# Kernel optimization log

Measured on AMD Instinct MI355X. Metric: run time of the kernel, lower is better.

The kernel has to match this reference:

```python
import jax, jax.numpy as jnp
import numpy as np

D_MODEL = 1024
N_HEADS = 16
D_HEAD = 64


def setup_inputs() -> dict:
    key = jax.random.key(0)
    ks = jax.random.split(key, 5)
    B, T = 2, 2048
    scale = 1.0 / np.sqrt(D_MODEL)
    x = jax.random.normal(ks[0], (B, T, D_MODEL), dtype=jnp.float32)
    Wq = jax.random.normal(ks[1], (N_HEADS * D_HEAD, D_MODEL), dtype=jnp.float32) * scale
    Wk = jax.random.normal(ks[2], (N_HEADS * D_HEAD, D_MODEL), dtype=jnp.float32) * scale
    Wv = jax.random.normal(ks[3], (N_HEADS * D_HEAD, D_MODEL), dtype=jnp.float32) * scale
    Wo = jax.random.normal(ks[4], (D_MODEL, N_HEADS * D_HEAD), dtype=jnp.float32) * scale
    return {"x": x, "Wq": Wq, "Wk": Wk, "Wv": Wv, "Wo": Wo}


def reference(x, Wq, Wk, Wv, Wo):
    B, T, D = x.shape
    # Linear(y = x @ W.T), then split heads: [B, H, T, d]
    def split_heads(y):
        return y.reshape(B, T, N_HEADS, D_HEAD).transpose(0, 2, 1, 3)
    q = split_heads(x @ Wq.T)
    k = split_heads(x @ Wk.T)
    v = split_heads(x @ Wv.T)
    scale = D_HEAD ** -0.5
    # Materialized [B, H, T, T] scores, as in the original module
    scores = jnp.einsum('bhtd,bhTd->bhtT', q, k) * scale
    attn = jax.nn.softmax(scores, axis=-1)
    y = jnp.einsum('bhtT,bhTd->bhtd', attn, v)
    y = y.transpose(0, 2, 1, 3).reshape(B, T, N_HEADS * D_HEAD)
    return y @ Wo.T
```

## Files before the change

### kernel.cpp

```cpp
#include <hip/hip_runtime.h>
#include <hip/hip_bf16.h>

typedef __attribute__((ext_vector_type(8))) short bf16x8;
typedef __attribute__((ext_vector_type(4))) float f32x4;
typedef unsigned short u16t;

#define DEVINL static __device__ __forceinline__

DEVINL u16t f2bf(float f) {
  union { __hip_bfloat16 h; u16t u; } cv;
  cv.h = __float2bfloat16(f);
  return cv.u;
}

DEVINL unsigned cvt_pk_bf16(float a, float b) {
  unsigned r;
  asm("v_cvt_pk_bf16_f32 %0, %1, %2" : "=v"(r) : "v"(a), "v"(b));
  return r;
}

DEVINL void async16(void* lds, const void* g) {
  __builtin_amdgcn_global_load_lds((const __attribute__((address_space(1))) void*)g,
                                   (__attribute__((address_space(3))) void*)lds,
                                   16, 0, 0);
}

__global__ __launch_bounds__(256) void convert_bf16(
    const float* __restrict__ x,  const float* __restrict__ wq,
    const float* __restrict__ wk, const float* __restrict__ wv,
    const float* __restrict__ wo,
    u16t* __restrict__ xb, u16t* __restrict__ wqb, u16t* __restrict__ wkb,
    u16t* __restrict__ wvb, u16t* __restrict__ wob) {
  const int blk = blockIdx.x;
  const float* src; u16t* dst; size_t off;
  if (blk < 4096)      { src = x;  dst = xb;  off = (size_t)blk * 1024; }
  else if (blk < 5120) { src = wq; dst = wqb; off = (size_t)(blk - 4096) * 1024; }
  else if (blk < 6144) { src = wk; dst = wkb; off = (size_t)(blk - 5120) * 1024; }
  else if (blk < 7168) { src = wv; dst = wvb; off = (size_t)(blk - 6144) * 1024; }
  else                 { src = wo; dst = wob; off = (size_t)(blk - 7168) * 1024; }
  const size_t i = off + (size_t)threadIdx.x * 4;
  const float4 v = *(const float4*)&src[i];
  ushort4 r;
  r.x = f2bf(v.x); r.y = f2bf(v.y); r.z = f2bf(v.z); r.w = f2bf(v.w);
  *(ushort4*)&dst[i] = r;
}

template <int MODE, int BM>
__global__ __launch_bounds__(256) void gemm_bt(
    const u16t* __restrict__ A, const u16t* __restrict__ B,
    void* __restrict__ C0, void* __restrict__ C1, void* __restrict__ C2,
    int M, int N, int K) {
  constexpr int MI = BM / 32;
  __shared__ u16t As[2][BM * 32];
  __shared__ u16t Bs[2][128 * 32];

  const int tid = threadIdx.x;
  const int lane = tid & 63;
  const int w = tid >> 6;
  const int wm = w >> 1, wn = w & 1;
  const int quad = lane >> 4, cl = lane & 15;
  const int m0 = blockIdx.y * BM;
  const int n0 = blockIdx.x * 128;

  const int srow = lane >> 2;
  const int scol = (lane & 3) * 8;

  f32x4 acc[MI][4] = {};

  #define STAGEP(b, kp)                                                       \
    {                                                                         \
      _Pragma("unroll")                                                       \
      for (int ii = 0; ii < BM / 64; ++ii) {                                  \
        const int c = w + ii * 4;                                             \
        async16(&As[b][c * 512],                                              \
                &A[(size_t)(m0 + c * 16 + srow) * K + (kp) * 32 + scol]);     \
      }                                                                       \
      _Pragma("unroll")                                                       \
      for (int ii = 0; ii < 2; ++ii) {                                        \
        const int c = w + ii * 4;                                             \
        async16(&Bs[b][c * 512],                                              \
                &B[(size_t)(n0 + c * 16 + srow) * K + (kp) * 32 + scol]);     \
      }                                                                       \
    }

  #define COMPUTEP(b)                                                         \
    {                                                                         \
      bf16x8 af[MI], bfr[4];                                                  \
      _Pragma("unroll")                                                       \
      for (int i = 0; i < MI; ++i)                                            \
        af[i] = *(const bf16x8*)&As[b][(wm * (BM / 2) + i * 16 + cl) * 32 + quad * 8]; \
      _Pragma("unroll")                                                       \
      for (int j = 0; j < 4; ++j)                                             \
        bfr[j] = *(const bf16x8*)&Bs[b][(wn * 64 + j * 16 + cl) * 32 + quad * 8]; \
      _Pragma("unroll")                                                       \
      for (int i = 0; i < MI; ++i)                                            \
        _Pragma("unroll")                                                     \
        for (int j = 0; j < 4; ++j)                                           \
          acc[i][j] = __builtin_amdgcn_mfma_f32_16x16x32_bf16(af[i], bfr[j], acc[i][j], 0, 0, 0); \
    }

  const int NP = K >> 5;
  STAGEP(0, 0);
  __syncthreads();
  for (int kp = 0; kp < NP; kp += 2) {
    if (kp + 1 < NP) STAGEP(1, kp + 1);
    COMPUTEP(0);
    __syncthreads();
    if (kp + 2 < NP) STAGEP(0, kp + 2);
    COMPUTEP(1);
    __syncthreads();
  }
  #undef STAGEP
  #undef COMPUTEP

  const int nz = n0 >> 10;
  #pragma unroll
  for (int i = 0; i < MI; ++i)
    #pragma unroll
    for (int j = 0; j < 4; ++j) {
      const int mb = m0 + wm * (BM / 2) + i * 16 + quad * 4;
      const int n  = n0 + wn * 64 + j * 16 + cl;
      if (MODE == 0) {
        #pragma unroll
        for (int r = 0; r < 4; ++r)
          ((float*)C0)[(size_t)(mb + r) * N + n] = acc[i][j][r];
      } else {
        const int nw = n & 1023, h = nw >> 6, d = nw & 63;
        const int b = mb >> 11, tb = mb & 2047;
        const size_t bh = (size_t)(b * 16 + h);
        if (nz == 2) {
          ushort4 v4;
          v4.x = f2bf(acc[i][j][0]); v4.y = f2bf(acc[i][j][1]);
          v4.z = f2bf(acc[i][j][2]); v4.w = f2bf(acc[i][j][3]);
          const size_t addr = (bh << 17) +
              (size_t)(((d >> 4) * 256 + (tb >> 3)) * 128 + (d & 15) * 8 + (tb & 7));
          *(ushort4*)&((u16t*)C2)[addr] = v4;
        } else if (nz == 1) {
          const size_t basea = (bh << 17) +
              (size_t)(((tb >> 4) * 8 + (d >> 3)) * 128 + (d & 7));
          #pragma unroll
          for (int r = 0; r < 4; ++r)
            ((u16t*)C1)[basea + ((tb & 15) + r) * 8] = f2bf(acc[i][j][r]);
        } else {
          #pragma unroll
          for (int r = 0; r < 4; ++r)
            ((u16t*)C0)[(bh * 2048 + tb + r) * 64 + d] =
                f2bf(acc[i][j][r] * 0.18033688011112043f);
        }
      }
    }
}

__global__ __launch_bounds__(256, 2) void flash_attn(
    const u16t* __restrict__ Q, const u16t* __restrict__ Kt,
    const u16t* __restrict__ Vt, u16t* __restrict__ Y) {
  __shared__ u16t Ps[4 * 32 * 136];
  const int tid = threadIdx.x;
  const int lane = tid & 63;
  const int w = tid >> 6;
  const int quad = lane >> 4, cl = lane & 15;
  const int bh = blockIdx.x;
  const int q0 = blockIdx.y * 128 + w * 32;
  const u16t* Kb = Kt + ((size_t)bh << 17);
  const u16t* Vb = Vt + ((size_t)bh << 17);

  bf16x8 aq[2][2];
  #pragma unroll
  for (int h = 0; h < 2; ++h)
    #pragma unroll
    for (int ks = 0; ks < 2; ++ks)
      aq[h][ks] = *(const bf16x8*)&Q[((size_t)bh * 2048 + q0 + 16 * h + cl) * 64 + ks * 32 + quad * 8];

  bf16x8 ones8;
  #pragma unroll
  for (int i = 0; i < 8; ++i) ones8[i] = (short)0x3F80;

  f32x4 o[2][4] = {};
  f32x4 psum[2] = {};

  u16t* Pw = &Ps[w * 32 * 136];

  for (int jt = 0; jt < 16; ++jt) {
    const int j0 = jt * 128;

    bf16x8 kf[2][8];
    #pragma unroll
    for (int ks = 0; ks < 2; ++ks)
      #pragma unroll
      for (int js = 0; js < 8; ++js)
        kf[ks][js] = *(const bf16x8*)&Kb[(size_t)((((j0 >> 4) + js) * 8 + ks * 4) * 128) + lane * 8];
    __builtin_amdgcn_sched_barrier(0);

    f32x4 s0[8] = {}, s1[8] = {};
    __builtin_amdgcn_s_setprio(1);
    #pragma unroll
    for (int ks = 0; ks < 2; ++ks) {
      #pragma unroll
      for (int js = 0; js < 8; ++js)
        s0[js] = __builtin_amdgcn_mfma_f32_16x16x32_bf16(kf[ks][js], aq[0][ks], s0[js], 0, 0, 0);
      #pragma unroll
      for (int js = 0; js < 8; ++js)
        s1[js] = __builtin_amdgcn_mfma_f32_16x16x32_bf16(kf[ks][js], aq[1][ks], s1[js], 0, 0, 0);
    }
    __builtin_amdgcn_s_setprio(0);

    bf16x8 vf[4][4];
    #pragma unroll
    for (int ks = 0; ks < 4; ++ks)
      #pragma unroll
      for (int ds = 0; ds < 4; ++ds)
        vf[ks][ds] = *(const bf16x8*)&Vb[(size_t)((ds * 256 + (j0 >> 3) + ks * 4) * 128) + lane * 8];
    __builtin_amdgcn_sched_barrier(0);

    #pragma unroll
    for (int js = 0; js < 8; ++js) {
      uint2 pk0, pk1;
      pk0.x = cvt_pk_bf16(__builtin_exp2f(s0[js][0]), __builtin_exp2f(s0[js][1]));
      pk0.y = cvt_pk_bf16(__builtin_exp2f(s0[js][2]), __builtin_exp2f(s0[js][3]));
      *(uint2*)&Pw[cl * 136 + js * 16 + quad * 4] = pk0;
      pk1.x = cvt_pk_bf16(__builtin_exp2f(s1[js][0]), __builtin_exp2f(s1[js][1]));
      pk1.y = cvt_pk_bf16(__builtin_exp2f(s1[js][2]), __builtin_exp2f(s1[js][3]));
      *(uint2*)&Pw[(16 + cl) * 136 + js * 16 + quad * 4] = pk1;
    }

    __builtin_amdgcn_s_setprio(1);
    #pragma unroll
    for (int ks = 0; ks < 4; ++ks) {
      const bf16x8 ap0 = *(const bf16x8*)&Pw[cl * 136 + ks * 32 + quad * 8];
      const bf16x8 ap1 = *(const bf16x8*)&Pw[(16 + cl) * 136 + ks * 32 + quad * 8];
      psum[0] = __builtin_amdgcn_mfma_f32_16x16x32_bf16(ap0, ones8, psum[0], 0, 0, 0);
      psum[1] = __builtin_amdgcn_mfma_f32_16x16x32_bf16(ap1, ones8, psum[1], 0, 0, 0);
      #pragma unroll
      for (int ds = 0; ds < 4; ++ds) {
        o[0][ds] = __builtin_amdgcn_mfma_f32_16x16x32_bf16(ap0, vf[ks][ds], o[0][ds], 0, 0, 0);
        o[1][ds] = __builtin_amdgcn_mfma_f32_16x16x32_bf16(ap1, vf[ks][ds], o[1][ds], 0, 0, 0);
      }
    }
    __builtin_amdgcn_s_setprio(0);
  }

  const int b = bh >> 4, hd = bh & 15;
  #pragma unroll
  for (int h = 0; h < 2; ++h) {
    float inv[4];
    #pragma unroll
    for (int r = 0; r < 4; ++r) inv[r] = __builtin_amdgcn_rcpf(psum[h][r]);
    #pragma unroll
    for (int ds = 0; ds < 4; ++ds)
      #pragma unroll
      for (int r = 0; r < 4; ++r) {
        const int t = q0 + 16 * h + quad * 4 + r;
        const int d = ds * 16 + cl;
        Y[((size_t)b * 2048 + t) * 1024 + hd * 64 + d] = f2bf(o[h][ds][r] * inv[r]);
      }
  }
}

extern "C" void kernel_launch(void* const* d_in, const int* in_sizes, int n_in,
                              void* d_out, int out_size, void* d_ws, size_t ws_size,
                              hipStream_t stream) {
  (void)in_sizes; (void)n_in; (void)out_size; (void)ws_size;
  const float* x  = (const float*)d_in[0];
  const float* Wq = (const float*)d_in[1];
  const float* Wk = (const float*)d_in[2];
  const float* Wv = (const float*)d_in[3];
  const float* Wo = (const float*)d_in[4];

  char* ws = (char*)d_ws;
  const size_t MB = 1024 * 1024;
  u16t* xb  = (u16t*)(ws);
  u16t* Wqb = (u16t*)(ws + 8 * MB);
  u16t* Wkb = (u16t*)(ws + 10 * MB);
  u16t* Wvb = (u16t*)(ws + 12 * MB);
  u16t* Wob = (u16t*)(ws + 14 * MB);
  u16t* Qw  = (u16t*)(ws + 16 * MB);
  u16t* Ktw = (u16t*)(ws + 24 * MB);
  u16t* Vtw = (u16t*)(ws + 32 * MB);
  u16t* Yw  = xb;

  convert_bf16<<<8192, 256, 0, stream>>>(x, Wq, Wk, Wv, Wo, xb, Wqb, Wkb, Wvb, Wob);
  gemm_bt<1, 128><<<dim3(24, 32), 256, 0, stream>>>(
      xb, Wqb, Qw, Ktw, Vtw, 4096, 3072, 1024);
  flash_attn<<<dim3(32, 16), 256, 0, stream>>>(Qw, Ktw, Vtw, Yw);
  gemm_bt<0, 64><<<dim3(8, 64), 256, 0, stream>>>(
      Yw, Wob, d_out, d_out, d_out, 4096, 1024, 1024);
}
```

Baseline: 196.1 us.

## Pre-swizzle QKV GEMM operands into fragment layout and load directly without LDS

The conversion kernel now writes x and the concatenated Wq/Wk/Wv in a 16-row by 8-element tiled layout that matches the MFMA fragment order, and does more work per block. A new QKV GEMM kernel reads its fragments straight from global memory with 16-byte loads, with no LDS staging or barriers, and asks for higher occupancy through its launch bounds. This removes shared-memory traffic and synchronization from the projection GEMM, but it relies on L1/L2 caching to supply operand reuse and has no software prefetch across k-steps.

```diff
diff --git a/kernel.cpp b/kernel.cpp
--- a/kernel.cpp
+++ b/kernel.cpp
@@ -2,6 +2,7 @@
 #include <hip/hip_bf16.h>
 
 typedef __attribute__((ext_vector_type(8))) short bf16x8;
+typedef __attribute__((ext_vector_type(8))) unsigned short u16x8;
 typedef __attribute__((ext_vector_type(4))) float f32x4;
 typedef unsigned short u16t;
 
@@ -29,20 +30,104 @@
     const float* __restrict__ x,  const float* __restrict__ wq,
     const float* __restrict__ wk, const float* __restrict__ wv,
     const float* __restrict__ wo,
-    u16t* __restrict__ xb, u16t* __restrict__ wqb, u16t* __restrict__ wkb,
-    u16t* __restrict__ wvb, u16t* __restrict__ wob) {
+    u16t* __restrict__ xb, u16t* __restrict__ wqb, u16t* __restrict__ wob) {
   const int blk = blockIdx.x;
-  const float* src; u16t* dst; size_t off;
-  if (blk < 4096)      { src = x;  dst = xb;  off = (size_t)blk * 1024; }
-  else if (blk < 5120) { src = wq; dst = wqb; off = (size_t)(blk - 4096) * 1024; }
-  else if (blk < 6144) { src = wk; dst = wkb; off = (size_t)(blk - 5120) * 1024; }
-  else if (blk < 7168) { src = wv; dst = wvb; off = (size_t)(blk - 6144) * 1024; }
-  else                 { src = wo; dst = wob; off = (size_t)(blk - 7168) * 1024; }
-  const size_t i = off + (size_t)threadIdx.x * 4;
-  const float4 v = *(const float4*)&src[i];
-  ushort4 r;
-  r.x = f2bf(v.x); r.y = f2bf(v.y); r.z = f2bf(v.z); r.w = f2bf(v.w);
-  *(ushort4*)&dst[i] = r;
+  const int tid = threadIdx.x;
+  if (blk < 896) {
+    const int lane = tid & 63, w = tid >> 6;
+    const int r = lane & 15, cw = lane >> 4;
+    int mg, half, row0;
+    const float* src; u16t* dst;
+    if (blk < 512) { mg = blk >> 1; half = blk & 1; src = x; dst = xb; row0 = mg * 16; }
+    else {
+      const int wblk = blk - 512;
+      mg = wblk >> 1; half = wblk & 1; dst = wqb;
+      const int n0 = mg * 16;
+      if (n0 < 1024)      { src = wq; row0 = n0; }
+      else if (n0 < 2048) { src = wk; row0 = n0 - 1024; }
+      else                { src = wv; row0 = n0 - 2048; }
+    }
+    #pragma unroll
+    for (int ic = 0; ic < 4; ++ic) {
+      const int c2 = half * 64 + w * 16 + ic * 4 + cw;
+      const float4 v0 = *(const float4*)&src[(size_t)(row0 + r) * 1024 + c2 * 8];
+      const float4 v1 = *(const float4*)&src[(size_t)(row0 + r) * 1024 + c2 * 8 + 4];
+      u16x8 o;
+      o[0] = f2bf(v0.x); o[1] = f2bf(v0.y); o[2] = f2bf(v0.z); o[3] = f2bf(v0.w);
+      o[4] = f2bf(v1.x); o[5] = f2bf(v1.y); o[6] = f2bf(v1.z); o[7] = f2bf(v1.w);
+      *(u16x8*)&dst[((size_t)mg * 128 + c2) * 128 + r * 8] = o;
+    }
+  } else {
+    const int row = blk - 896;
+    const size_t i = (size_t)row * 1024 + (size_t)tid * 4;
+    const float4 v = *(const float4*)&wo[i];
+    ushort4 rr;
+    rr.x = f2bf(v.x); rr.y = f2bf(v.y); rr.z = f2bf(v.z); rr.w = f2bf(v.w);
+    *(ushort4*)&wob[i] = rr;
+  }
+}
+
+__global__ __launch_bounds__(256, 4) void gemm_fs(
+    const u16t* __restrict__ A, const u16t* __restrict__ B,
+    void* __restrict__ C0, void* __restrict__ C1, void* __restrict__ C2) {
+  const int tid = threadIdx.x;
+  const int lane = tid & 63;
+  const int w = tid >> 6;
+  const int wm = w >> 1, wn = w & 1;
+  const int quad = lane >> 4, cl = lane & 15;
+  const int m0 = blockIdx.y * 128;
+  const int n0 = blockIdx.x * 128;
+
+  const u16t* Ap = A + ((size_t)((m0 >> 4) + wm * 4) * 128 + quad) * 128 + cl * 8;
+  const u16t* Bp = B + ((size_t)((n0 >> 4) + wn * 4) * 128 + quad) * 128 + cl * 8;
+
+  f32x4 acc[4][4] = {};
+  #pragma unroll 1
+  for (int kp = 0; kp < 32; ++kp) {
+    bf16x8 af[4], bfr[4];
+    #pragma unroll
+    for (int i = 0; i < 4; ++i)
+      af[i] = *(const bf16x8*)&Ap[(size_t)i * 16384 + kp * 512];
+    #pragma unroll
+    for (int j = 0; j < 4; ++j)
+      bfr[j] = *(const bf16x8*)&Bp[(size_t)j * 16384 + kp * 512];
+    #pragma unroll
+    for (int i = 0; i < 4; ++i)
+      #pragma unroll
+      for (int j = 0; j < 4; ++j)
+        acc[i][j] = __builtin_amdgcn_mfma_f32_16x16x32_bf16(af[i], bfr[j], acc[i][j], 0, 0, 0);
+  }
+
+  const int nz = n0 >> 10;
+  #pragma unroll
+  for (int i = 0; i < 4; ++i)
+    #pragma unroll
+    for (int j = 0; j < 4; ++j) {
+      const int mb = m0 + wm * 64 + i * 16 + quad * 4;
+      const int n  = n0 + wn * 64 + j * 16 + cl;
+      const int nw = n & 1023, h = nw >> 6, d = nw & 63;
+      const int b = mb >> 11, tb = mb & 2047;
+      const size_t bh = (size_t)(b * 16 + h);
+      if (nz == 2) {
+        ushort4 v4;
+        v4.x = f2bf(acc[i][j][0]); v4.y = f2bf(acc[i][j][1]);
+        v4.z = f2bf(acc[i][j][2]); v4.w = f2bf(acc[i][j][3]);
+        const size_t addr = (bh << 17) +
+            (size_t)(((d >> 4) * 256 + (tb >> 3)) * 128 + (d & 15) * 8 + (tb & 7));
+        *(ushort4*)&((u16t*)C2)[addr] = v4;
+      } else if (nz == 1) {
+        const size_t basea = (bh << 17) +
+            (size_t)(((tb >> 4) * 8 + (d >> 3)) * 128 + (d & 7));
+        #pragma unroll
+        for (int r = 0; r < 4; ++r)
+          ((u16t*)C1)[basea + ((tb & 15) + r) * 8] = f2bf(acc[i][j][r]);
+      } else {
+        #pragma unroll
+        for (int r = 0; r < 4; ++r)
+          ((u16t*)C0)[(bh * 2048 + tb + r) * 64 + d] =
+              f2bf(acc[i][j][r] * 0.18033688011112043f);
+      }
+    }
 }
 
 template <int MODE, int BM>
@@ -113,7 +198,6 @@
   #undef STAGEP
   #undef COMPUTEP
 
-  const int nz = n0 >> 10;
   #pragma unroll
   for (int i = 0; i < MI; ++i)
     #pragma unroll
@@ -124,30 +208,8 @@
         #pragma unroll
         for (int r = 0; r < 4; ++r)
           ((float*)C0)[(size_t)(mb + r) * N + n] = acc[i][j][r];
-      } else {
-        const int nw = n & 1023, h = nw >> 6, d = nw & 63;
-        const int b = mb >> 11, tb = mb & 2047;
-        const size_t bh = (size_t)(b * 16 + h);
-        if (nz == 2) {
-          ushort4 v4;
-          v4.x = f2bf(acc[i][j][0]); v4.y = f2bf(acc[i][j][1]);
-          v4.z = f2bf(acc[i][j][2]); v4.w = f2bf(acc[i][j][3]);
-          const size_t addr = (bh << 17) +
-              (size_t)(((d >> 4) * 256 + (tb >> 3)) * 128 + (d & 15) * 8 + (tb & 7));
-          *(ushort4*)&((u16t*)C2)[addr] = v4;
-        } else if (nz == 1) {
-          const size_t basea = (bh << 17) +
-              (size_t)(((tb >> 4) * 8 + (d >> 3)) * 128 + (d & 7));
-          #pragma unroll
-          for (int r = 0; r < 4; ++r)
-            ((u16t*)C1)[basea + ((tb & 15) + r) * 8] = f2bf(acc[i][j][r]);
-        } else {
-          #pragma unroll
-          for (int r = 0; r < 4; ++r)
-            ((u16t*)C0)[(bh * 2048 + tb + r) * 64 + d] =
-                f2bf(acc[i][j][r] * 0.18033688011112043f);
-        }
       }
+      (void)C1; (void)C2;
     }
 }
 
@@ -270,17 +332,14 @@
   const size_t MB = 1024 * 1024;
   u16t* xb  = (u16t*)(ws);
   u16t* Wqb = (u16t*)(ws + 8 * MB);
-  u16t* Wkb = (u16t*)(ws + 10 * MB);
-  u16t* Wvb = (u16t*)(ws + 12 * MB);
   u16t* Wob = (u16t*)(ws + 14 * MB);
   u16t* Qw  = (u16t*)(ws + 16 * MB);
   u16t* Ktw = (u16t*)(ws + 24 * MB);
   u16t* Vtw = (u16t*)(ws + 32 * MB);
   u16t* Yw  = xb;
 
-  convert_bf16<<<8192, 256, 0, stream>>>(x, Wq, Wk, Wv, Wo, xb, Wqb, Wkb, Wvb, Wob);
-  gemm_bt<1, 128><<<dim3(24, 32), 256, 0, stream>>>(
-      xb, Wqb, Qw, Ktw, Vtw, 4096, 3072, 1024);
+  convert_bf16<<<1920, 256, 0, stream>>>(x, Wq, Wk, Wv, Wo, xb, Wqb, Wob);
+  gemm_fs<<<dim3(24, 32), 256, 0, stream>>>(xb, Wqb, Qw, Ktw, Vtw);
   flash_attn<<<dim3(32, 16), 256, 0, stream>>>(Qw, Ktw, Vtw, Yw);
   gemm_bt<0, 64><<<dim3(8, 64), 256, 0, stream>>>(
       Yw, Wob, d_out, d_out, d_out, 4096, 1024, 1024);
```

New measurement: 191.7 us. 2.2% less time.
